# Performance work log

Hardware: AMD Instinct MI355X
Metric: run time of the kernel (lower is better)

Reference implementation:

```python
import jax, jax.numpy as jnp
import numpy as np
from functools import partial

EPS = 1e-5
ROPE_THETA = 10000.0
TOP_K = 2


def rmsnorm(x, w):
    # x: [..., d]
    var = jnp.mean(x * x, axis=-1, keepdims=True)
    return x * jax.lax.rsqrt(var + EPS) * w


def apply_rope(x):
    # x: [B, S, H, dh]
    B, S, H, dh = x.shape
    inv_freq = 1.0 / (ROPE_THETA ** (jnp.arange(0, dh, 2, dtype=jnp.float32) / dh))
    ang = jnp.arange(S, dtype=jnp.float32)[:, None] * inv_freq[None, :]  # [S, dh/2]
    cos = jnp.cos(ang)[None, :, None, :]
    sin = jnp.sin(ang)[None, :, None, :]
    x1 = x[..., 0::2]
    x2 = x[..., 1::2]
    r1 = x1 * cos - x2 * sin
    r2 = x1 * sin + x2 * cos
    return jnp.stack([r1, r2], axis=-1).reshape(x.shape)


def setup_inputs() -> dict:
    key = jax.random.key(0)
    B, S, D, H, E = 4, 2048, 512, 8, 8
    Hf = 4 * D  # expert FFN hidden
    ks = jax.random.split(key, 10)
    s = 0.02
    return {
        "x": jax.random.normal(ks[0], (B, S, D), dtype=jnp.float32),
        "attn_norm_w": jnp.ones((D,), dtype=jnp.float32),
        "wq": jax.random.normal(ks[1], (D, D), dtype=jnp.float32) * s,
        "wk": jax.random.normal(ks[2], (D, D), dtype=jnp.float32) * s,
        "wv": jax.random.normal(ks[3], (D, D), dtype=jnp.float32) * s,
        "wo": jax.random.normal(ks[4], (D, D), dtype=jnp.float32) * s,
        "ffn_norm_w": jnp.ones((D,), dtype=jnp.float32),
        "router_w": jax.random.normal(ks[5], (D, E), dtype=jnp.float32) * s,
        "w1": jax.random.normal(ks[6], (E, D, Hf), dtype=jnp.float32) * s,
        "w2": jax.random.normal(ks[7], (E, Hf, D), dtype=jnp.float32) * s,
    }


def mha_rope(xn, wq, wk, wv, wo, num_heads):
    B, S, D = xn.shape
    dh = D // num_heads
    q = (xn @ wq).reshape(B, S, num_heads, dh)
    k = (xn @ wk).reshape(B, S, num_heads, dh)
    v = (xn @ wv).reshape(B, S, num_heads, dh)
    q = apply_rope(q)
    k = apply_rope(k)
    scores = jnp.einsum("bqhd,bkhd->bhqk", q, k) / jnp.sqrt(jnp.float32(dh))
    causal = jnp.tril(jnp.ones((S, S), dtype=bool))
    scores = jnp.where(causal[None, None], scores, jnp.float32(-1e9))
    attn = jax.nn.softmax(scores, axis=-1)
    out = jnp.einsum("bhqk,bkhd->bqhd", attn, v).reshape(B, S, D)
    return out @ wo


def moe_ffn(hn, router_w, w1, w2):
    # hn: [B, S, D] -> tokens [T, D]; top-2 routed expert MLPs (GELU)
    B, S, D = hn.shape
    E = router_w.shape[1]
    t = hn.reshape(B * S, D)
    T = t.shape[0]
    logits = t @ router_w                      # [T, E]
    probs = jax.nn.softmax(logits, axis=-1)
    vals, idx = jax.lax.top_k(probs, TOP_K)    # [T, k]
    gates = vals / jnp.sum(vals, axis=-1, keepdims=True)
    gates_dense = jnp.zeros((T, E), dtype=t.dtype).at[
        jnp.arange(T)[:, None], idx
    ].add(gates)                               # sparse gates, zero for unrouted
    out = jnp.zeros_like(t)
    for e in range(E):  # fixed small expert loop
        ge = gates_dense[:, e:e + 1]           # [T, 1]
        h = jax.nn.gelu(t @ w1[e], approximate=False)
        out = out + ge * (h @ w2[e])
    return out.reshape(B, S, D)


def reference(x, attn_norm_w, wq, wk, wv, wo, ffn_norm_w, router_w, w1, w2):
    num_heads = 8
    h = x + mha_rope(rmsnorm(x, attn_norm_w), wq, wk, wv, wo, num_heads)
    out = h + moe_ffn(rmsnorm(h, ffn_norm_w), router_w, w1, w2)
    return out
```

## Files before the change

kernel.cpp:

```cpp
#include <hip/hip_runtime.h>

#define BATCH 4
#define SEQ 2048
#define DMODEL 512
#define NHEAD 8
#define DHEAD 64
#define NEXP 8
#define DFF 2048
#define TOK (BATCH*SEQ)

typedef __attribute__((ext_vector_type(8))) short short8;
typedef __attribute__((ext_vector_type(8))) _Float16 half8;
typedef __attribute__((ext_vector_type(4))) float f32x4;
typedef unsigned short u16;

typedef const __attribute__((address_space(1))) void gvoid;
typedef __attribute__((address_space(3))) void lvoid;
__device__ __forceinline__ void gload16(const void* g, void* l){
  __builtin_amdgcn_global_load_lds((gvoid*)g, (lvoid*)l, 16, 0, 0);
}

__device__ inline f32x4 zero4(){ f32x4 z = {0.f,0.f,0.f,0.f}; return z; }
__device__ inline u16 f2bf(float f){ unsigned u; __builtin_memcpy(&u,&f,4); u = (u + 0x7fffu + ((u>>16)&1u)) >> 16; return (u16)u; }
__device__ inline unsigned pack2(_Float16 a, _Float16 b){
  unsigned short ua, ub; __builtin_memcpy(&ua,&a,2); __builtin_memcpy(&ub,&b,2);
  return (unsigned)ua | ((unsigned)ub<<16);
}

__global__ __launch_bounds__(256) void k_tc_bf(const float* __restrict__ W, u16* __restrict__ Wt, int R, int C){
  __shared__ float tile[32][33];
  long e = blockIdx.z;
  const float* Wp = W + e*(long)R*C;
  u16* Op = Wt + e*(long)R*C;
  int c0 = blockIdx.x*32, r0 = blockIdx.y*32;
  int tx = threadIdx.x & 31, ty = threadIdx.x >> 5;
  #pragma unroll
  for (int i=0;i<4;i++){ int r = ty*4+i; tile[r][tx] = Wp[(long)(r0+r)*C + c0+tx]; }
  __syncthreads();
  #pragma unroll
  for (int i=0;i<4;i++){ int cc = ty*4+i; Op[(long)(c0+cc)*R + r0+tx] = f2bf(tile[tx][cc]); }
}

__global__ __launch_bounds__(256) void k_tc_split(const float* __restrict__ W, _Float16* __restrict__ H, _Float16* __restrict__ L, int R, int C){
  __shared__ float tile[32][33];
  int c0 = blockIdx.x*32, r0 = blockIdx.y*32;
  int tx = threadIdx.x & 31, ty = threadIdx.x >> 5;
  #pragma unroll
  for (int i=0;i<4;i++){ int r = ty*4+i; tile[r][tx] = W[(long)(r0+r)*C + c0+tx]; }
  __syncthreads();
  #pragma unroll
  for (int i=0;i<4;i++){
    int cc = ty*4+i;
    float v = tile[tx][cc];
    _Float16 hi = (_Float16)v;
    long o = (long)(c0+cc)*R + r0+tx;
    H[o] = hi; L[o] = (_Float16)(v - (float)hi);
  }
}

__global__ __launch_bounds__(256) void k_vtrans(const _Float16* __restrict__ vh, const _Float16* __restrict__ vl,
                                                _Float16* __restrict__ vth, _Float16* __restrict__ vtl){
  __shared__ _Float16 t[32][33];
  int bh = blockIdx.z;
  int b = bh>>3, h = bh&7;
  int s0 = blockIdx.x*32, d0 = blockIdx.y*32;
  int tx = threadIdx.x & 31, ty = threadIdx.x >> 5;
  const _Float16* src = vh; _Float16* dst = vth;
  #pragma unroll
  for (int pass=0; pass<2; pass++){
    #pragma unroll
    for (int i=0;i<4;i++){
      int sl = ty*4+i;
      t[sl][tx] = src[((long)b*SEQ + s0+sl)*DMODEL + h*64 + d0 + tx];
    }
    __syncthreads();
    #pragma unroll
    for (int i=0;i<4;i++){
      int dl = ty*4+i;
      dst[((long)bh*64 + d0+dl)*SEQ + s0 + tx] = t[tx][dl];
    }
    __syncthreads();
    src = vl; dst = vtl;
  }
}

__global__ __launch_bounds__(256) void k_rmsnorm_split(const float* __restrict__ x, const float* __restrict__ w,
                                                       _Float16* __restrict__ oh, _Float16* __restrict__ ol){
  int row = blockIdx.x*4 + (threadIdx.x>>6);
  int lane = threadIdx.x & 63;
  const float4* xr = (const float4*)(x + (long)row*DMODEL);
  float4 a = xr[lane*2], b = xr[lane*2+1];
  float ss = a.x*a.x+a.y*a.y+a.z*a.z+a.w*a.w + b.x*b.x+b.y*b.y+b.z*b.z+b.w*b.w;
  #pragma unroll
  for (int o=32;o;o>>=1) ss += __shfl_xor(ss, o);
  float sc = rsqrtf(ss*(1.0f/DMODEL) + 1e-5f);
  const float4* wr = (const float4*)w;
  float4 wa = wr[lane*2], wb = wr[lane*2+1];
  float v[8] = {a.x*sc*wa.x, a.y*sc*wa.y, a.z*sc*wa.z, a.w*sc*wa.w,
                b.x*sc*wb.x, b.y*sc*wb.y, b.z*sc*wb.z, b.w*sc*wb.w};
  half8 hv, lv;
  #pragma unroll
  for (int j=0;j<8;j++){ _Float16 hi = (_Float16)v[j]; hv[j] = hi; lv[j] = (_Float16)(v[j]-(float)hi); }
  long off = (long)row*DMODEL + lane*8;
  *(half8*)(oh + off) = hv;
  *(half8*)(ol + off) = lv;
}

__global__ __launch_bounds__(256) void k_rmsnorm_bf(const float* __restrict__ x, const float* __restrict__ w, u16* __restrict__ o){
  int row = blockIdx.x*4 + (threadIdx.x>>6);
  int lane = threadIdx.x & 63;
  const float4* xr = (const float4*)(x + (long)row*DMODEL);
  float4 a = xr[lane*2], b = xr[lane*2+1];
  float ss = a.x*a.x+a.y*a.y+a.z*a.z+a.w*a.w + b.x*b.x+b.y*b.y+b.z*b.z+b.w*b.w;
  #pragma unroll
  for (int ofs=32;ofs;ofs>>=1) ss += __shfl_xor(ss, ofs);
  float sc = rsqrtf(ss*(1.0f/DMODEL) + 1e-5f);
  const float4* wr = (const float4*)w;
  float4 wa = wr[lane*2], wb = wr[lane*2+1];
  short8 ov;
  ov[0]=(short)f2bf(a.x*sc*wa.x); ov[1]=(short)f2bf(a.y*sc*wa.y);
  ov[2]=(short)f2bf(a.z*sc*wa.z); ov[3]=(short)f2bf(a.w*sc*wa.w);
  ov[4]=(short)f2bf(b.x*sc*wb.x); ov[5]=(short)f2bf(b.y*sc*wb.y);
  ov[6]=(short)f2bf(b.z*sc*wb.z); ov[7]=(short)f2bf(b.w*sc*wb.w);
  *(short8*)(o + (long)row*DMODEL + lane*8) = ov;
}

__global__ __launch_bounds__(256) void k_rope_tab(float2* __restrict__ tab){
  int idx = blockIdx.x*256 + threadIdx.x;
  int s = idx>>5, i = idx&31;
  float invf = powf(10000.0f, -(float)(2*i)*(1.0f/64.0f));
  float ang = (float)s * invf;
  tab[idx] = make_float2(cosf(ang), sinf(ang));
}

template<int EPI>
__global__ __launch_bounds__(256) void k_gemm_split(
    const _Float16* __restrict__ Ah, const _Float16* __restrict__ Al,
    const _Float16* __restrict__ Bh, const _Float16* __restrict__ Bl,
    _Float16* __restrict__ oh, _Float16* __restrict__ ol,
    float* __restrict__ of1, float* __restrict__ of2,
    const float* __restrict__ extra, const float2* __restrict__ tab,
    int M, int N, int K)
{
  __shared__ _Float16 lAb[2*128*64];
  __shared__ _Float16 lBb[2*128*64];
  const int mb = blockIdx.x*128, nb = blockIdx.y*128;
  const int tid = threadIdx.x, lane = tid&63, wv = tid>>6;
  const int wr = wv>>1, wc = wv&1;
  const int fr = lane&15, fq = lane>>4;
  const int cs = (lane&7) ^ (lane>>3);
  const _Float16* pA[4]; const _Float16* pB[4];
  #pragma unroll
  for (int i=0;i<4;i++){
    int rr = i*32 + wv*8 + (lane>>3);
    const _Float16* a = (cs<4)? Ah : Al;
    const _Float16* b = (cs<4)? Bh : Bl;
    pA[i] = a + (long)(mb+rr)*K + (cs&3)*8;
    pB[i] = b + (long)(nb+rr)*K + (cs&3)*8;
  }
  f32x4 acc[4][4];
  #pragma unroll
  for (int mi=0;mi<4;mi++)
    #pragma unroll
    for (int ni=0;ni<4;ni++) acc[mi][ni] = zero4();

  #pragma unroll
  for (int i=0;i<4;i++){
    gload16(pA[i], (char*)lAb + (i*32+wv*8)*128);
    gload16(pB[i], (char*)lBb + (i*32+wv*8)*128);
  }
  __syncthreads();
  const int NT = K>>5;
  int cur = 0;
  for (int t=0; t<NT; ++t){
    if (t+1 < NT){
      int k2 = (t+1)<<5;
      #pragma unroll
      for (int i=0;i<4;i++){
        int db = ((cur^1)<<14) + (i*32+wv*8)*128;
        gload16(pA[i]+k2, (char*)lAb + db);
        gload16(pB[i]+k2, (char*)lBb + db);
      }
    }
    const char* cA = (const char*)lAb + (cur<<14);
    const char* cB = (const char*)lBb + (cur<<14);
    half8 ax[4], ay[4], bx[4], by[4];
    #pragma unroll
    for (int mi=0;mi<4;mi++){
      int row = wr*64 + mi*16 + fr; int m7 = row&7; const char* rb = cA + row*128;
      ax[mi] = *(const half8*)(rb + (((fq  ) ^ m7)<<4));
      ay[mi] = *(const half8*)(rb + (((fq+4) ^ m7)<<4));
    }
    #pragma unroll
    for (int ni=0;ni<4;ni++){
      int row = wc*64 + ni*16 + fr; int m7 = row&7; const char* rb = cB + row*128;
      bx[ni] = *(const half8*)(rb + (((fq  ) ^ m7)<<4));
      by[ni] = *(const half8*)(rb + (((fq+4) ^ m7)<<4));
    }
    __builtin_amdgcn_s_setprio(1);
    #pragma unroll
    for (int mi=0;mi<4;mi++)
      #pragma unroll
      for (int ni=0;ni<4;ni++){
        acc[mi][ni] = __builtin_amdgcn_mfma_f32_16x16x32_f16(ax[mi], bx[ni], acc[mi][ni], 0,0,0);
        acc[mi][ni] = __builtin_amdgcn_mfma_f32_16x16x32_f16(ax[mi], by[ni], acc[mi][ni], 0,0,0);
        acc[mi][ni] = __builtin_amdgcn_mfma_f32_16x16x32_f16(ay[mi], bx[ni], acc[mi][ni], 0,0,0);
      }
    __builtin_amdgcn_s_setprio(0);
    __syncthreads();
    cur ^= 1;
  }
  #pragma unroll
  for (int mi=0;mi<4;mi++)
    #pragma unroll
    for (int ni=0;ni<4;ni++)
      #pragma unroll
      for (int r=0;r<4;r++){
        int row = mb + wr*64 + mi*16 + fq*4 + r;
        int col = nb + wc*64 + ni*16 + fr;
        long off = (long)row*N + col;
        float v = acc[mi][ni][r];
        if (EPI==0){
          float v2 = __shfl_xor(v, 1);
          float2 csn = tab[(row & (SEQ-1))*32 + ((col&63)>>1)];
          float o = (col&1) ? (v2*csn.y + v*csn.x) : (v*csn.x - v2*csn.y);
          _Float16 hi = (_Float16)o;
          oh[off] = hi; ol[off] = (_Float16)(o - (float)hi);
        } else if (EPI==1){
          _Float16 hi = (_Float16)v;
          oh[off] = hi; ol[off] = (_Float16)(v - (float)hi);
        } else {
          float hv = extra[off] + v;
          of1[off] = hv; of2[off] = hv;
        }
      }
}

__global__ __launch_bounds__(256) void k_flash(
    const _Float16* __restrict__ Qh, const _Float16* __restrict__ Ql,
    const _Float16* __restrict__ Kh, const _Float16* __restrict__ Kl,
    const _Float16* __restrict__ Vth, const _Float16* __restrict__ Vtl,
    _Float16* __restrict__ Oh, _Float16* __restrict__ Ol)
{
  __shared__ _Float16 lK[64*128];
  __shared__ _Float16 lV[64*128];
  __shared__ _Float16 lP[4*2304];
  const int pidx = blockIdx.x, bh = blockIdx.y;
  const int b = bh>>3, hh = bh&7;
  const int tid = threadIdx.x, lane = tid&63, wid = tid>>6;
  const int fr = lane&15, fq = lane>>4;
  const long base = ((long)b*SEQ)*DMODEL + hh*DHEAD;
  const long vtb  = (long)bh*DHEAD*SEQ;
  const int srow = tid>>4, sch = tid&15;
  const unsigned pw = wid*2304;
  const float SCL = 0.18033688011112042f;

  half8 kreg[4], vreg[4];
  const _Float16* ks = (sch<8) ? Kh : Kl;
  const _Float16* vs = (sch<8) ? Vth : Vtl;
  #pragma unroll
  for (int i=0;i<4;i++){
    int row = i*16 + srow;
    kreg[i] = *(const half8*)(ks + base + (long)row*DMODEL + (sch&7)*8);
    vreg[i] = *(const half8*)(vs + vtb + (long)row*SEQ + (sch&7)*8);
  }

  for (int pass=0; pass<2; pass++){
    const int qt = pass ? (SEQ/64-1-pidx) : pidx;
    const int q0 = qt*64, qw = q0 + wid*16;
    half8 qfh[2], qfl[2];
    #pragma unroll
    for (int kk=0;kk<2;kk++){
      long o = base + (long)(qw+fr)*DMODEL + kk*32 + fq*8;
      qfh[kk] = *(const half8*)(Qh + o);
      qfl[kk] = *(const half8*)(Ql + o);
    }
    f32x4 oacc[4];
    #pragma unroll
    for (int i=0;i<4;i++) oacc[i] = zero4();
    float mrow[4], lrow[4];
    #pragma unroll
    for (int r=0;r<4;r++){ mrow[r] = -__builtin_inff(); lrow[r] = 0.f; }

    for (int kvt=0; kvt<=qt; kvt++){
      int k0 = kvt*64;
      __syncthreads();
      #pragma unroll
      for (int i=0;i<4;i++){
        int row = i*16 + srow;
        int slot = ((sch ^ (row&15))<<4);
        *(half8*)((char*)lK + row*256 + slot) = kreg[i];
        *(half8*)((char*)lV + row*256 + slot) = vreg[i];
      }
      __syncthreads();
      {
        int nk0 = -1;
        if (kvt < qt) nk0 = k0 + 64;
        else if (pass == 0) nk0 = 0;
        if (nk0 >= 0){
          #pragma unroll
          for (int i=0;i<4;i++){
            int row = i*16 + srow;
            kreg[i] = *(const half8*)(ks + base + (long)(nk0+row)*DMODEL + (sch&7)*8);
            vreg[i] = *(const half8*)(vs + vtb + (long)row*SEQ + nk0 + (sch&7)*8);
          }
        }
      }
      f32x4 sc[4];
      __builtin_amdgcn_s_setprio(1);
      #pragma unroll
      for (int ns=0;ns<4;ns++){
        f32x4 a = zero4();
        #pragma unroll
        for (int kk=0;kk<2;kk++){
          int row = ns*16 + fr; int m15 = row&15; const char* rb = (const char*)lK + row*256;
          half8 kfh = *(const half8*)(rb + (((kk*4+fq)   ^ m15)<<4));
          half8 kfl = *(const half8*)(rb + (((kk*4+fq+8) ^ m15)<<4));
          a = __builtin_amdgcn_mfma_f32_16x16x32_f16(qfh[kk], kfh, a, 0,0,0);
          a = __builtin_amdgcn_mfma_f32_16x16x32_f16(qfh[kk], kfl, a, 0,0,0);
          a = __builtin_amdgcn_mfma_f32_16x16x32_f16(qfl[kk], kfh, a, 0,0,0);
        }
        sc[ns] = a;
      }
      __builtin_amdgcn_s_setprio(0);
      float pmax[4];
      #pragma unroll
      for (int r=0;r<4;r++) pmax[r] = -__builtin_inff();
      if (kvt == qt){
        #pragma unroll
        for (int ns=0;ns<4;ns++)
          #pragma unroll
          for (int r=0;r<4;r++){
            int kvp = k0 + ns*16 + fr;
            int qp  = qw + fq*4 + r;
            float s = sc[ns][r]*SCL;
            if (kvp > qp) s = -1e30f;
            sc[ns][r] = s;
            pmax[r] = fmaxf(pmax[r], s);
          }
      } else {
        #pragma unroll
        for (int ns=0;ns<4;ns++)
          #pragma unroll
          for (int r=0;r<4;r++){
            float s = sc[ns][r]*SCL;
            sc[ns][r] = s;
            pmax[r] = fmaxf(pmax[r], s);
          }
      }
      #pragma unroll
      for (int o=1;o<16;o<<=1)
        #pragma unroll
        for (int r=0;r<4;r++) pmax[r] = fmaxf(pmax[r], __shfl_xor(pmax[r], o));
      bool need = false;
      #pragma unroll
      for (int r=0;r<4;r++) need = need || (pmax[r] > mrow[r] + 10.f);
      if (__any(need)){
        float sf[4];
        #pragma unroll
        for (int r=0;r<4;r++){
          float mn = fmaxf(mrow[r], pmax[r]);
          sf[r] = exp2f(mrow[r]-mn);
          mrow[r] = mn;
          lrow[r] *= sf[r];
        }
        #pragma unroll
        for (int dt=0;dt<4;dt++)
          #pragma unroll
          for (int r=0;r<4;r++) oacc[dt][r] *= sf[r];
      }
      float rsum[4] = {0,0,0,0};
      #pragma unroll
      for (int ns=0;ns<4;ns++)
        #pragma unroll
        for (int r=0;r<4;r++){
          float pv = exp2f(sc[ns][r]-mrow[r]);
          rsum[r] += pv;
          float pv2 = __shfl_xor(pv, 1);
          float e0 = (fr&1)? pv2 : pv;
          float e1 = (fr&1)? pv : pv2;
          _Float16 f0 = (_Float16)e0, f1 = (_Float16)e1;
          unsigned word;
          if (fr&1) word = pack2((_Float16)(e0-(float)f0), (_Float16)(e1-(float)f1));
          else      word = pack2(f0, f1);
          unsigned eo = pw + ((fr&1)? 1152u:0u) + (unsigned)((fq*4+r)*72 + ns*16 + (fr&~1));
          *(unsigned*)((char*)lP + eo*2) = word;
        }
      #pragma unroll
      for (int o=1;o<16;o<<=1)
        #pragma unroll
        for (int r=0;r<4;r++) rsum[r] += __shfl_xor(rsum[r], o);
      #pragma unroll
      for (int r=0;r<4;r++) lrow[r] += rsum[r];
      __builtin_amdgcn_s_setprio(1);
      #pragma unroll
      for (int kk=0;kk<2;kk++){
        const char* pb = (const char*)lP + (pw + (unsigned)(fr*72 + kk*32))*2;
        half8 pfh = *(const half8*)(pb + fq*16);
        half8 pfl = *(const half8*)(pb + 2304 + fq*16);
        #pragma unroll
        for (int dt=0;dt<4;dt++){
          int row = dt*16 + fr; int m15 = row&15; const char* vb = (const char*)lV + row*256;
          half8 vfh = *(const half8*)(vb + (((kk*4+fq)   ^ m15)<<4));
          half8 vfl = *(const half8*)(vb + (((kk*4+fq+8) ^ m15)<<4));
          oacc[dt] = __builtin_amdgcn_mfma_f32_16x16x32_f16(pfh, vfh, oacc[dt], 0,0,0);
          oacc[dt] = __builtin_amdgcn_mfma_f32_16x16x32_f16(pfh, vfl, oacc[dt], 0,0,0);
          oacc[dt] = __builtin_amdgcn_mfma_f32_16x16x32_f16(pfl, vfh, oacc[dt], 0,0,0);
        }
      }
      __builtin_amdgcn_s_setprio(0);
    }
    #pragma unroll
    for (int dt=0;dt<4;dt++)
      #pragma unroll
      for (int r=0;r<4;r++){
        int qp = qw + fq*4 + r;
        float ov = oacc[dt][r] / lrow[r];
        long o = base + (long)qp*DMODEL + dt*16 + fr;
        _Float16 hi = (_Float16)ov;
        Oh[o] = hi; Ol[o] = (_Float16)(ov - (float)hi);
      }
  }
}

__global__ __launch_bounds__(256) void k_router(const float* __restrict__ h, const float* __restrict__ w,
                                                const float* __restrict__ rw, float* __restrict__ gates,
                                                unsigned* __restrict__ choice){
  int tok = blockIdx.x*4 + (threadIdx.x>>6);
  int lane = threadIdx.x & 63;
  const float4* xr = (const float4*)(h + (long)tok*DMODEL);
  float4 a = xr[lane*2], b = xr[lane*2+1];
  float ss = a.x*a.x+a.y*a.y+a.z*a.z+a.w*a.w + b.x*b.x+b.y*b.y+b.z*b.z+b.w*b.w;
  #pragma unroll
  for (int o=32;o;o>>=1) ss += __shfl_xor(ss, o);
  float sc = rsqrtf(ss*(1.0f/DMODEL) + 1e-5f);
  const float4* wr = (const float4*)w;
  float4 wa = wr[lane*2], wb = wr[lane*2+1];
  float xv[8] = {a.x*sc*wa.x, a.y*sc*wa.y, a.z*sc*wa.z, a.w*sc*wa.w,
                 b.x*sc*wb.x, b.y*sc*wb.y, b.z*sc*wb.z, b.w*sc*wb.w};
  float lg[8] = {0,0,0,0,0,0,0,0};
  #pragma unroll
  for (int j=0;j<8;j++){
    const float* rp = rw + (long)(lane*8+j)*NEXP;
    #pragma unroll
    for (int e=0;e<8;e++) lg[e] += xv[j]*rp[e];
  }
  #pragma unroll
  for (int o=1;o<64;o<<=1)
    #pragma unroll
    for (int e=0;e<8;e++) lg[e] += __shfl_xor(lg[e], o);
  float mx = lg[0];
  #pragma unroll
  for (int e=1;e<8;e++) mx = fmaxf(mx, lg[e]);
  float pe[8], sm = 0.f;
  #pragma unroll
  for (int e=0;e<8;e++){ pe[e] = expf(lg[e]-mx); sm += pe[e]; }
  #pragma unroll
  for (int e=0;e<8;e++) pe[e] /= sm;
  int e1 = 0; float p1 = pe[0];
  #pragma unroll
  for (int e=1;e<8;e++) if (pe[e] > p1){ p1 = pe[e]; e1 = e; }
  int e2 = -1; float p2 = -1.f;
  #pragma unroll
  for (int e=0;e<8;e++) if (e != e1 && pe[e] > p2){ p2 = pe[e]; e2 = e; }
  float gs = p1 + p2;
  if (lane == 0){
    #pragma unroll
    for (int e=0;e<8;e++)
      gates[(long)tok*NEXP + e] = (e==e1) ? (p1/gs) : ((e==e2) ? (p2/gs) : 0.f);
    choice[tok] = (unsigned)e1 | ((unsigned)e2<<8);
  }
}

__global__ __launch_bounds__(256) void k_build(const unsigned* __restrict__ choice,
                                               int* __restrict__ cnt, int* __restrict__ perm){
  __shared__ int lcnt[NEXP];
  __shared__ int lbase[NEXP];
  const int tid = threadIdx.x;
  const int tok = blockIdx.x*256 + tid;
  if (tid < NEXP) lcnt[tid] = 0;
  __syncthreads();
  unsigned ch = choice[tok];
  int e1 = ch & 0xff, e2 = (ch>>8) & 0xff;
  int p1 = atomicAdd(&lcnt[e1], 1);
  int p2 = atomicAdd(&lcnt[e2], 1);
  __syncthreads();
  if (tid < NEXP) lbase[tid] = atomicAdd(&cnt[tid], lcnt[tid]);
  __syncthreads();
  perm[e1*TOK + lbase[e1] + p1] = tok;
  perm[e2*TOK + lbase[e2] + p2] = tok;
}

__global__ void k_prefix(const int* __restrict__ cnt, int* __restrict__ baseP){
  if (threadIdx.x==0 && blockIdx.x==0){
    int run = 0;
    for (int e=0;e<NEXP;e++){ baseP[e] = run; run += (cnt[e]+127) & ~127; }
  }
}

__global__ __launch_bounds__(256) void k_moe1(
    const u16* __restrict__ A, const u16* __restrict__ W1, u16* __restrict__ mid,
    const int* __restrict__ perm, const int* __restrict__ cnt, const int* __restrict__ baseP)
{
  const int e = blockIdx.z;
  const int ce = cnt[e];
  const int mb = blockIdx.x*128;
  if (mb >= ce) return;
  const int bp = baseP[e];
  const u16* Bt = W1 + (size_t)e*DFF*DMODEL;
  const int nb = blockIdx.y*128;
  __shared__ u16 lA[128*64];
  __shared__ u16 lB[128*64];
  const int tid = threadIdx.x, lane = tid&63, wv = tid>>6;
  const int wr = wv>>1, wc = wv&1;
  const int fr = lane&15, fq = lane>>4;
  const int cs = (lane&7) ^ (lane>>3);
  const u16* pA[4]; const u16* pB[4];
  #pragma unroll
  for (int i=0;i<4;i++){
    int rr = mb + i*32 + wv*8 + (lane>>3);
    int tok = perm[e*TOK + (rr < ce ? rr : ce-1)];
    pA[i] = A  + (long)tok*DMODEL + cs*8;
    pB[i] = Bt + (long)(nb + i*32 + wv*8 + (lane>>3))*DMODEL + cs*8;
  }
  f32x4 acc[4][4];
  #pragma unroll
  for (int mi=0;mi<4;mi++)
    #pragma unroll
    for (int ni=0;ni<4;ni++) acc[mi][ni] = zero4();

  for (int kt=0; kt<DMODEL; kt+=64){
    #pragma unroll
    for (int i=0;i<4;i++){
      gload16(pA[i]+kt, (char*)lA + (i*32+wv*8)*128);
      gload16(pB[i]+kt, (char*)lB + (i*32+wv*8)*128);
    }
    __syncthreads();
    __builtin_amdgcn_s_setprio(1);
    #pragma unroll
    for (int kk=0;kk<2;kk++){
      short8 af[4], bff[4];
      #pragma unroll
      for (int mi=0;mi<4;mi++){
        int row = wr*64 + mi*16 + fr;
        af[mi] = *(const short8*)((char*)lA + row*128 + (((kk*4+fq) ^ (row&7))<<4));
      }
      #pragma unroll
      for (int ni=0;ni<4;ni++){
        int row = wc*64 + ni*16 + fr;
        bff[ni] = *(const short8*)((char*)lB + row*128 + (((kk*4+fq) ^ (row&7))<<4));
      }
      #pragma unroll
      for (int mi=0;mi<4;mi++)
        #pragma unroll
        for (int ni=0;ni<4;ni++)
          acc[mi][ni] = __builtin_amdgcn_mfma_f32_16x16x32_bf16(af[mi], bff[ni], acc[mi][ni], 0,0,0);
    }
    __builtin_amdgcn_s_setprio(0);
    __syncthreads();
  }
  #pragma unroll
  for (int mi=0;mi<4;mi++)
    #pragma unroll
    for (int ni=0;ni<4;ni++)
      #pragma unroll
      for (int r=0;r<4;r++){
        int row_loc = mb + wr*64 + mi*16 + fq*4 + r;
        int col = nb + wc*64 + ni*16 + fr;
        float v = acc[mi][ni][r];
        mid[(size_t)(bp + row_loc)*DFF + col] = f2bf(0.5f*v*(1.f + erff(v*0.7071067811865475f)));
      }
}

__global__ __launch_bounds__(256) void k_moe2(
    const u16* __restrict__ mid, const u16* __restrict__ W2, float* __restrict__ out,
    const int* __restrict__ perm, const int* __restrict__ cnt, const int* __restrict__ baseP,
    const float* __restrict__ gates)
{
  const int e = blockIdx.z;
  const int ce = cnt[e];
  const int mb = blockIdx.x*128;
  if (mb >= ce) return;
  const int bp = baseP[e];
  const u16* Bt = W2 + (size_t)e*DMODEL*DFF;
  const int nb = blockIdx.y*128;
  __shared__ u16 lA[128*64];
  __shared__ u16 lB[128*64];
  const int tid = threadIdx.x, lane = tid&63, wv = tid>>6;
  const int wr = wv>>1, wc = wv&1;
  const int fr = lane&15, fq = lane>>4;
  const int cs = (lane&7) ^ (lane>>3);
  const u16* pA[4]; const u16* pB[4];
  #pragma unroll
  for (int i=0;i<4;i++){
    int rr = i*32 + wv*8 + (lane>>3);
    pA[i] = mid + (size_t)(bp + mb + rr)*DFF + cs*8;
    pB[i] = Bt  + (long)(nb + rr)*DFF + cs*8;
  }
  f32x4 acc[4][4];
  #pragma unroll
  for (int mi=0;mi<4;mi++)
    #pragma unroll
    for (int ni=0;ni<4;ni++) acc[mi][ni] = zero4();

  for (int kt=0; kt<DFF; kt+=64){
    #pragma unroll
    for (int i=0;i<4;i++){
      gload16(pA[i]+kt, (char*)lA + (i*32+wv*8)*128);
      gload16(pB[i]+kt, (char*)lB + (i*32+wv*8)*128);
    }
    __syncthreads();
    __builtin_amdgcn_s_setprio(1);
    #pragma unroll
    for (int kk=0;kk<2;kk++){
      short8 af[4], bff[4];
      #pragma unroll
      for (int mi=0;mi<4;mi++){
        int row = wr*64 + mi*16 + fr;
        af[mi] = *(const short8*)((char*)lA + row*128 + (((kk*4+fq) ^ (row&7))<<4));
      }
      #pragma unroll
      for (int ni=0;ni<4;ni++){
        int row = wc*64 + ni*16 + fr;
        bff[ni] = *(const short8*)((char*)lB + row*128 + (((kk*4+fq) ^ (row&7))<<4));
      }
      #pragma unroll
      for (int mi=0;mi<4;mi++)
        #pragma unroll
        for (int ni=0;ni<4;ni++)
          acc[mi][ni] = __builtin_amdgcn_mfma_f32_16x16x32_bf16(af[mi], bff[ni], acc[mi][ni], 0,0,0);
    }
    __builtin_amdgcn_s_setprio(0);
    __syncthreads();
  }
  #pragma unroll
  for (int mi=0;mi<4;mi++)
    #pragma unroll
    for (int ni=0;ni<4;ni++)
      #pragma unroll
      for (int r=0;r<4;r++){
        int row_loc = mb + wr*64 + mi*16 + fq*4 + r;
        if (row_loc < ce){
          int tok = perm[e*TOK + row_loc];
          int col = nb + wc*64 + ni*16 + fr;
          float g = gates[(long)tok*NEXP + e];
          atomicAdd(out + (long)tok*DMODEL + col, g*acc[mi][ni][r]);
        }
      }
}

extern "C" void kernel_launch(void* const* d_in, const int* in_sizes, int n_in,
                              void* d_out, int out_size, void* d_ws, size_t ws_size,
                              hipStream_t stream)
{
  const float* x   = (const float*)d_in[0];
  const float* anw = (const float*)d_in[1];
  const float* wq  = (const float*)d_in[2];
  const float* wk  = (const float*)d_in[3];
  const float* wv  = (const float*)d_in[4];
  const float* wo  = (const float*)d_in[5];
  const float* fnw = (const float*)d_in[6];
  const float* rw  = (const float*)d_in[7];
  const float* w1  = (const float*)d_in[8];
  const float* w2  = (const float*)d_in[9];
  float* out = (float*)d_out;

  char* p = (char*)d_ws;
  auto alloc = [&](size_t n){ char* r = p; p += (n + 255) & ~(size_t)255; return r; };
  _Float16* xnh = (_Float16*)alloc((size_t)TOK*DMODEL*2);
  _Float16* xnl = (_Float16*)alloc((size_t)TOK*DMODEL*2);
  _Float16* qh  = (_Float16*)alloc((size_t)TOK*DMODEL*2);
  _Float16* ql  = (_Float16*)alloc((size_t)TOK*DMODEL*2);
  _Float16* kh  = (_Float16*)alloc((size_t)TOK*DMODEL*2);
  _Float16* kl  = (_Float16*)alloc((size_t)TOK*DMODEL*2);
  _Float16* vh  = (_Float16*)alloc((size_t)TOK*DMODEL*2);
  _Float16* vl  = (_Float16*)alloc((size_t)TOK*DMODEL*2);
  _Float16* vth = (_Float16*)alloc((size_t)TOK*DMODEL*2);
  _Float16* vtl = (_Float16*)alloc((size_t)TOK*DMODEL*2);
  u16* hmid = (u16*)xnh;
  _Float16* wqTh = (_Float16*)alloc((size_t)DMODEL*DMODEL*2);
  _Float16* wqTl = (_Float16*)alloc((size_t)DMODEL*DMODEL*2);
  _Float16* wkTh = (_Float16*)alloc((size_t)DMODEL*DMODEL*2);
  _Float16* wkTl = (_Float16*)alloc((size_t)DMODEL*DMODEL*2);
  _Float16* wvTh = (_Float16*)alloc((size_t)DMODEL*DMODEL*2);
  _Float16* wvTl = (_Float16*)alloc((size_t)DMODEL*DMODEL*2);
  _Float16* woTh = (_Float16*)alloc((size_t)DMODEL*DMODEL*2);
  _Float16* woTl = (_Float16*)alloc((size_t)DMODEL*DMODEL*2);
  u16* w1T = (u16*)alloc((size_t)NEXP*DFF*DMODEL*2);
  u16* w2T = (u16*)alloc((size_t)NEXP*DMODEL*DFF*2);
  _Float16* aoh = (_Float16*)alloc((size_t)TOK*DMODEL*2);
  _Float16* aol = (_Float16*)alloc((size_t)TOK*DMODEL*2);
  float* hb  = (float*)alloc((size_t)TOK*DMODEL*4);
  u16* hnb   = (u16*)alloc((size_t)TOK*DMODEL*2);
  float2* tab = (float2*)alloc((size_t)SEQ*32*sizeof(float2));
  float* gates = (float*)alloc((size_t)TOK*NEXP*4);
  int* perm  = (int*)alloc((size_t)NEXP*TOK*4);
  unsigned* choice = (unsigned*)alloc((size_t)TOK*4);
  int* cnt   = (int*)alloc(64*4);
  int* baseP = (int*)alloc(64*4);

  dim3 blk(256);
  hipMemsetAsync(cnt, 0, NEXP*sizeof(int), stream);
  k_tc_split<<<dim3(16,16,1), blk, 0, stream>>>(wq, wqTh, wqTl, DMODEL, DMODEL);
  k_tc_split<<<dim3(16,16,1), blk, 0, stream>>>(wk, wkTh, wkTl, DMODEL, DMODEL);
  k_tc_split<<<dim3(16,16,1), blk, 0, stream>>>(wv, wvTh, wvTl, DMODEL, DMODEL);
  k_tc_split<<<dim3(16,16,1), blk, 0, stream>>>(wo, woTh, woTl, DMODEL, DMODEL);
  k_tc_bf<<<dim3(DFF/32, DMODEL/32, NEXP), blk, 0, stream>>>(w1, w1T, DMODEL, DFF);
  k_tc_bf<<<dim3(DMODEL/32, DFF/32, NEXP), blk, 0, stream>>>(w2, w2T, DFF, DMODEL);
  k_rope_tab<<<dim3(SEQ*32/256), blk, 0, stream>>>(tab);
  k_rmsnorm_split<<<dim3(TOK/4), blk, 0, stream>>>(x, anw, xnh, xnl);
  k_gemm_split<0><<<dim3(TOK/128, DMODEL/128), blk, 0, stream>>>(xnh, xnl, wqTh, wqTl, qh, ql, nullptr, nullptr, nullptr, tab, TOK, DMODEL, DMODEL);
  k_gemm_split<0><<<dim3(TOK/128, DMODEL/128), blk, 0, stream>>>(xnh, xnl, wkTh, wkTl, kh, kl, nullptr, nullptr, nullptr, tab, TOK, DMODEL, DMODEL);
  k_gemm_split<1><<<dim3(TOK/128, DMODEL/128), blk, 0, stream>>>(xnh, xnl, wvTh, wvTl, vh, vl, nullptr, nullptr, nullptr, nullptr, TOK, DMODEL, DMODEL);
  k_vtrans<<<dim3(SEQ/32, 2, BATCH*NHEAD), blk, 0, stream>>>(vh, vl, vth, vtl);
  k_flash<<<dim3(SEQ/128, BATCH*NHEAD), blk, 0, stream>>>(qh, ql, kh, kl, vth, vtl, aoh, aol);
  k_gemm_split<2><<<dim3(TOK/128, DMODEL/128), blk, 0, stream>>>(aoh, aol, woTh, woTl, nullptr, nullptr, hb, out, x, nullptr, TOK, DMODEL, DMODEL);
  k_router<<<dim3(TOK/4), blk, 0, stream>>>(hb, fnw, rw, gates, choice);
  k_build<<<dim3(TOK/256), blk, 0, stream>>>(choice, cnt, perm);
  k_prefix<<<dim3(1), dim3(64), 0, stream>>>(cnt, baseP);
  k_rmsnorm_bf<<<dim3(TOK/4), blk, 0, stream>>>(hb, fnw, hnb);
  k_moe1<<<dim3(TOK/128, DFF/128, NEXP), blk, 0, stream>>>(hnb, w1T, hmid, perm, cnt, baseP);
  k_moe2<<<dim3(TOK/128, DMODEL/128, NEXP), blk, 0, stream>>>(hmid, w2T, out, perm, cnt, baseP, gates);
}
```

Measured before the change: 672.7 us.

## Fuse V transpose into GEMM epilogue, fold FFN rmsnorm into router, split-K moe2

The V projection GEMM now writes its output directly in the per-head transposed layout, so the separate transpose kernel and its intermediate buffers go away. The router kernel also emits the bf16-normalized activations, which removes the standalone rmsnorm pass over h. The second MoE GEMM splits its K dimension in two, doubling the grid to improve occupancy. This relies on moe2 accumulating into the output atomically, and adds more atomic traffic.

```diff
diff --git a/kernel.cpp b/kernel.cpp
--- a/kernel.cpp
+++ b/kernel.cpp
@@ -11,6 +11,7 @@
 
 typedef __attribute__((ext_vector_type(8))) short short8;
 typedef __attribute__((ext_vector_type(8))) _Float16 half8;
+typedef __attribute__((ext_vector_type(4))) _Float16 half4;
 typedef __attribute__((ext_vector_type(4))) float f32x4;
 typedef unsigned short u16;
 
@@ -58,32 +59,6 @@
   }
 }
 
-__global__ __launch_bounds__(256) void k_vtrans(const _Float16* __restrict__ vh, const _Float16* __restrict__ vl,
-                                                _Float16* __restrict__ vth, _Float16* __restrict__ vtl){
-  __shared__ _Float16 t[32][33];
-  int bh = blockIdx.z;
-  int b = bh>>3, h = bh&7;
-  int s0 = blockIdx.x*32, d0 = blockIdx.y*32;
-  int tx = threadIdx.x & 31, ty = threadIdx.x >> 5;
-  const _Float16* src = vh; _Float16* dst = vth;
-  #pragma unroll
-  for (int pass=0; pass<2; pass++){
-    #pragma unroll
-    for (int i=0;i<4;i++){
-      int sl = ty*4+i;
-      t[sl][tx] = src[((long)b*SEQ + s0+sl)*DMODEL + h*64 + d0 + tx];
-    }
-    __syncthreads();
-    #pragma unroll
-    for (int i=0;i<4;i++){
-      int dl = ty*4+i;
-      dst[((long)bh*64 + d0+dl)*SEQ + s0 + tx] = t[tx][dl];
-    }
-    __syncthreads();
-    src = vl; dst = vtl;
-  }
-}
-
 __global__ __launch_bounds__(256) void k_rmsnorm_split(const float* __restrict__ x, const float* __restrict__ w,
                                                        _Float16* __restrict__ oh, _Float16* __restrict__ ol){
   int row = blockIdx.x*4 + (threadIdx.x>>6);
@@ -104,25 +79,6 @@
   long off = (long)row*DMODEL + lane*8;
   *(half8*)(oh + off) = hv;
   *(half8*)(ol + off) = lv;
-}
-
-__global__ __launch_bounds__(256) void k_rmsnorm_bf(const float* __restrict__ x, const float* __restrict__ w, u16* __restrict__ o){
-  int row = blockIdx.x*4 + (threadIdx.x>>6);
-  int lane = threadIdx.x & 63;
-  const float4* xr = (const float4*)(x + (long)row*DMODEL);
-  float4 a = xr[lane*2], b = xr[lane*2+1];
-  float ss = a.x*a.x+a.y*a.y+a.z*a.z+a.w*a.w + b.x*b.x+b.y*b.y+b.z*b.z+b.w*b.w;
-  #pragma unroll
-  for (int ofs=32;ofs;ofs>>=1) ss += __shfl_xor(ss, ofs);
-  float sc = rsqrtf(ss*(1.0f/DMODEL) + 1e-5f);
-  const float4* wr = (const float4*)w;
-  float4 wa = wr[lane*2], wb = wr[lane*2+1];
-  short8 ov;
-  ov[0]=(short)f2bf(a.x*sc*wa.x); ov[1]=(short)f2bf(a.y*sc*wa.y);
-  ov[2]=(short)f2bf(a.z*sc*wa.z); ov[3]=(short)f2bf(a.w*sc*wa.w);
-  ov[4]=(short)f2bf(b.x*sc*wb.x); ov[5]=(short)f2bf(b.y*sc*wb.y);
-  ov[6]=(short)f2bf(b.z*sc*wb.z); ov[7]=(short)f2bf(b.w*sc*wb.w);
-  *(short8*)(o + (long)row*DMODEL + lane*8) = ov;
 }
 
 __global__ __launch_bounds__(256) void k_rope_tab(float2* __restrict__ tab){
@@ -210,30 +166,49 @@
     __syncthreads();
     cur ^= 1;
   }
-  #pragma unroll
-  for (int mi=0;mi<4;mi++)
-    #pragma unroll
-    for (int ni=0;ni<4;ni++)
-      #pragma unroll
-      for (int r=0;r<4;r++){
-        int row = mb + wr*64 + mi*16 + fq*4 + r;
-        int col = nb + wc*64 + ni*16 + fr;
-        long off = (long)row*N + col;
-        float v = acc[mi][ni][r];
-        if (EPI==0){
-          float v2 = __shfl_xor(v, 1);
-          float2 csn = tab[(row & (SEQ-1))*32 + ((col&63)>>1)];
-          float o = (col&1) ? (v2*csn.y + v*csn.x) : (v*csn.x - v2*csn.y);
-          _Float16 hi = (_Float16)o;
-          oh[off] = hi; ol[off] = (_Float16)(o - (float)hi);
-        } else if (EPI==1){
+  if (EPI==1){
+    #pragma unroll
+    for (int mi=0;mi<4;mi++)
+      #pragma unroll
+      for (int ni=0;ni<4;ni++){
+        int row0 = mb + wr*64 + mi*16 + fq*4;
+        int col  = nb + wc*64 + ni*16 + fr;
+        int d = col & (DHEAD-1), hh = col >> 6;
+        int bb = row0 >> 11, s = row0 & (SEQ-1);
+        long to = ((long)(bb*NHEAD + hh)*DHEAD + d)*SEQ + s;
+        half4 hv, lv;
+        #pragma unroll
+        for (int r=0;r<4;r++){
+          float v = acc[mi][ni][r];
           _Float16 hi = (_Float16)v;
-          oh[off] = hi; ol[off] = (_Float16)(v - (float)hi);
-        } else {
-          float hv = extra[off] + v;
-          of1[off] = hv; of2[off] = hv;
+          hv[r] = hi; lv[r] = (_Float16)(v - (float)hi);
         }
-      }
+        *(half4*)(oh + to) = hv;
+        *(half4*)(ol + to) = lv;
+      }
+  } else {
+    #pragma unroll
+    for (int mi=0;mi<4;mi++)
+      #pragma unroll
+      for (int ni=0;ni<4;ni++)
+        #pragma unroll
+        for (int r=0;r<4;r++){
+          int row = mb + wr*64 + mi*16 + fq*4 + r;
+          int col = nb + wc*64 + ni*16 + fr;
+          long off = (long)row*N + col;
+          float v = acc[mi][ni][r];
+          if (EPI==0){
+            float v2 = __shfl_xor(v, 1);
+            float2 csn = tab[(row & (SEQ-1))*32 + ((col&63)>>1)];
+            float o = (col&1) ? (v2*csn.y + v*csn.x) : (v*csn.x - v2*csn.y);
+            _Float16 hi = (_Float16)o;
+            oh[off] = hi; ol[off] = (_Float16)(o - (float)hi);
+          } else {
+            float hv = extra[off] + v;
+            of1[off] = hv; of2[off] = hv;
+          }
+        }
+  }
 }
 
 __global__ __launch_bounds__(256) void k_flash(
@@ -425,7 +400,7 @@
 
 __global__ __launch_bounds__(256) void k_router(const float* __restrict__ h, const float* __restrict__ w,
                                                 const float* __restrict__ rw, float* __restrict__ gates,
-                                                unsigned* __restrict__ choice){
+                                                unsigned* __restrict__ choice, u16* __restrict__ hnb){
   int tok = blockIdx.x*4 + (threadIdx.x>>6);
   int lane = threadIdx.x & 63;
   const float4* xr = (const float4*)(h + (long)tok*DMODEL);
@@ -438,6 +413,10 @@
   float4 wa = wr[lane*2], wb = wr[lane*2+1];
   float xv[8] = {a.x*sc*wa.x, a.y*sc*wa.y, a.z*sc*wa.z, a.w*sc*wa.w,
                  b.x*sc*wb.x, b.y*sc*wb.y, b.z*sc*wb.z, b.w*sc*wb.w};
+  short8 ov;
+  #pragma unroll
+  for (int j=0;j<8;j++) ov[j] = (short)f2bf(xv[j]);
+  *(short8*)(hnb + (long)tok*DMODEL + lane*8) = ov;
   float lg[8] = {0,0,0,0,0,0,0,0};
   #pragma unroll
   for (int j=0;j<8;j++){
@@ -577,7 +556,8 @@
     const int* __restrict__ perm, const int* __restrict__ cnt, const int* __restrict__ baseP,
     const float* __restrict__ gates)
 {
-  const int e = blockIdx.z;
+  const int ez = blockIdx.z;
+  const int e = ez>>1, kh = ez&1;
   const int ce = cnt[e];
   const int mb = blockIdx.x*128;
   if (mb >= ce) return;
@@ -603,7 +583,8 @@
     #pragma unroll
     for (int ni=0;ni<4;ni++) acc[mi][ni] = zero4();
 
-  for (int kt=0; kt<DFF; kt+=64){
+  const int kbeg = kh*(DFF/2), kend = kbeg + DFF/2;
+  for (int kt=kbeg; kt<kend; kt+=64){
     #pragma unroll
     for (int i=0;i<4;i++){
       gload16(pA[i]+kt, (char*)lA + (i*32+wv*8)*128);
@@ -673,10 +654,11 @@
   _Float16* ql  = (_Float16*)alloc((size_t)TOK*DMODEL*2);
   _Float16* kh  = (_Float16*)alloc((size_t)TOK*DMODEL*2);
   _Float16* kl  = (_Float16*)alloc((size_t)TOK*DMODEL*2);
-  _Float16* vh  = (_Float16*)alloc((size_t)TOK*DMODEL*2);
-  _Float16* vl  = (_Float16*)alloc((size_t)TOK*DMODEL*2);
   _Float16* vth = (_Float16*)alloc((size_t)TOK*DMODEL*2);
   _Float16* vtl = (_Float16*)alloc((size_t)TOK*DMODEL*2);
+  _Float16* pad1 = (_Float16*)alloc((size_t)TOK*DMODEL*2);
+  _Float16* pad2 = (_Float16*)alloc((size_t)TOK*DMODEL*2);
+  (void)pad1; (void)pad2;
   u16* hmid = (u16*)xnh;
   _Float16* wqTh = (_Float16*)alloc((size_t)DMODEL*DMODEL*2);
   _Float16* wqTl = (_Float16*)alloc((size_t)DMODEL*DMODEL*2);
@@ -711,14 +693,12 @@
   k_rmsnorm_split<<<dim3(TOK/4), blk, 0, stream>>>(x, anw, xnh, xnl);
   k_gemm_split<0><<<dim3(TOK/128, DMODEL/128), blk, 0, stream>>>(xnh, xnl, wqTh, wqTl, qh, ql, nullptr, nullptr, nullptr, tab, TOK, DMODEL, DMODEL);
   k_gemm_split<0><<<dim3(TOK/128, DMODEL/128), blk, 0, stream>>>(xnh, xnl, wkTh, wkTl, kh, kl, nullptr, nullptr, nullptr, tab, TOK, DMODEL, DMODEL);
-  k_gemm_split<1><<<dim3(TOK/128, DMODEL/128), blk, 0, stream>>>(xnh, xnl, wvTh, wvTl, vh, vl, nullptr, nullptr, nullptr, nullptr, TOK, DMODEL, DMODEL);
-  k_vtrans<<<dim3(SEQ/32, 2, BATCH*NHEAD), blk, 0, stream>>>(vh, vl, vth, vtl);
+  k_gemm_split<1><<<dim3(TOK/128, DMODEL/128), blk, 0, stream>>>(xnh, xnl, wvTh, wvTl, vth, vtl, nullptr, nullptr, nullptr, nullptr, TOK, DMODEL, DMODEL);
   k_flash<<<dim3(SEQ/128, BATCH*NHEAD), blk, 0, stream>>>(qh, ql, kh, kl, vth, vtl, aoh, aol);
   k_gemm_split<2><<<dim3(TOK/128, DMODEL/128), blk, 0, stream>>>(aoh, aol, woTh, woTl, nullptr, nullptr, hb, out, x, nullptr, TOK, DMODEL, DMODEL);
-  k_router<<<dim3(TOK/4), blk, 0, stream>>>(hb, fnw, rw, gates, choice);
+  k_router<<<dim3(TOK/4), blk, 0, stream>>>(hb, fnw, rw, gates, choice, hnb);
   k_build<<<dim3(TOK/256), blk, 0, stream>>>(choice, cnt, perm);
   k_prefix<<<dim3(1), dim3(64), 0, stream>>>(cnt, baseP);
-  k_rmsnorm_bf<<<dim3(TOK/4), blk, 0, stream>>>(hb, fnw, hnb);
   k_moe1<<<dim3(TOK/128, DFF/128, NEXP), blk, 0, stream>>>(hnb, w1T, hmid, perm, cnt, baseP);
-  k_moe2<<<dim3(TOK/128, DMODEL/128, NEXP), blk, 0, stream>>>(hmid, w2T, out, perm, cnt, baseP, gates);
-}
+  k_moe2<<<dim3(TOK/128, DMODEL/128, NEXP*2), blk, 0, stream>>>(hmid, w2T, out, perm, cnt, baseP, gates);
+}
```

Measured after the change: 752.9 us. 11.9% more time.
